# Performance work log

Hardware: AMD Instinct MI355X
Metric: run time of the kernel (lower is better)

The kernel has to match this reference:

```python
import jax, jax.numpy as jnp
import numpy as np

N = 5000
E = 160000
H = 6   # num_heads
D = 64  # out feats per head
IN = 131


def _gat_layer(h, W, al, ar, b, src, dst, activate):
    """DGL-style GATConv: fc -> edge attention -> edge softmax -> scatter sum."""
    n = h.shape[0]
    f = (h @ W).reshape(n, H, D)                      # [N,H,D]
    el = (f * al).sum(-1)                             # [N,H]
    er = (f * ar).sum(-1)                             # [N,H]
    e = jax.nn.leaky_relu(el[src] + er[dst], 0.2)     # [E,H]
    emax = jax.ops.segment_max(e, dst, num_segments=n)
    ex = jnp.exp(e - emax[dst])
    den = jax.ops.segment_sum(ex, dst, num_segments=n)
    alpha = ex / den[dst]                             # [E,H] edge softmax per dst
    out = jax.ops.segment_sum(f[src] * alpha[:, :, None], dst, num_segments=n)
    out = out + b.reshape(H, D)
    return jax.nn.elu(out) if activate else out


def setup_inputs() -> dict:
    ks = jax.random.split(jax.random.key(0), 24)
    s = 0.05
    inp = {
        "nfeats": jax.random.normal(ks[0], (N, IN), jnp.float32),
        "dis": jax.random.uniform(ks[1], (N, N), jnp.float32),
        "src": jax.random.randint(ks[2], (E,), 0, N),
        "dst": jax.random.randint(ks[3], (E,), 0, N),
    }
    dims_in = [IN, H * D, H * D, H * D]
    for l in range(4):
        inp[f"w{l}"] = jax.random.normal(ks[4 + 4 * l], (dims_in[l], H * D), jnp.float32) * s
        inp[f"al{l}"] = jax.random.normal(ks[5 + 4 * l], (H, D), jnp.float32) * s
        inp[f"ar{l}"] = jax.random.normal(ks[6 + 4 * l], (H, D), jnp.float32) * s
        inp[f"b{l}"] = jax.random.normal(ks[7 + 4 * l], (H * D,), jnp.float32) * s
    inp["pw"] = jax.random.normal(ks[20], (129,), jnp.float32) * s
    inp["pb"] = jax.random.normal(ks[21], (), jnp.float32) * s
    return inp


def reference(nfeats, dis, src, dst,
              w0, al0, ar0, b0, w1, al1, ar1, b1,
              w2, al2, ar2, b2, w3, al3, ar3, b3, pw, pb):
    n = nfeats.shape[0]
    h = nfeats
    h = _gat_layer(h, w0, al0, ar0, b0, src, dst, True).reshape(n, H * D)
    h = _gat_layer(h, w1, al1, ar1, b1, src, dst, True).reshape(n, H * D)
    h = _gat_layer(h, w2, al2, ar2, b2, src, dst, True).reshape(n, H * D)
    emb = _gat_layer(h, w3, al3, ar3, b3, src, dst, False).mean(axis=1)  # [N,64]
    # pair_emb[i,j] = [emb[j], emb[i], dis[i,j]] -> Linear(129,1) -> tanh
    s1 = emb @ pw[:D]        # coefficient on emb[j]
    s2 = emb @ pw[D:2 * D]   # coefficient on emb[i]
    OD = jnp.tanh(s2[:, None] + s1[None, :] + dis * pw[2 * D] + pb)
    return OD
```

## Files before the change

kernel.cpp:

```cpp
#include <hip/hip_runtime.h>
#include <math.h>

#define N_NODES 5000
#define E_EDGES 160000
#define H_HEADS 6
#define D_FEAT  64
#define IN_FEAT 131
#define HD      384
#define NC4     (N_NODES/4)
#define AGG_CAP 1024

typedef float vf4 __attribute__((ext_vector_type(4)));

__global__ void k_count(const int* __restrict__ dst, int* __restrict__ deg) {
    int e = blockIdx.x * blockDim.x + threadIdx.x;
    if (e < E_EDGES) atomicAdd(&deg[dst[e]], 1);
}

__global__ void k_scan(int* __restrict__ deg, int* __restrict__ row_ptr) {
    __shared__ int part[1024];
    const int T = 1024;
    int t = threadIdx.x;
    const int per = (N_NODES + T - 1) / T;
    int start = t * per;
    int s = 0;
    for (int i = 0; i < per; i++) {
        int idx = start + i;
        if (idx < N_NODES) s += deg[idx];
    }
    part[t] = s;
    __syncthreads();
    for (int off = 1; off < T; off <<= 1) {
        int v = (t >= off) ? part[t - off] : 0;
        __syncthreads();
        part[t] += v;
        __syncthreads();
    }
    int excl = (t == 0) ? 0 : part[t - 1];
    for (int i = 0; i < per; i++) {
        int idx = start + i;
        if (idx < N_NODES) {
            row_ptr[idx] = excl;
            excl += deg[idx];
            deg[idx] = 0;
        }
    }
    if (t == T - 1) row_ptr[N_NODES] = part[T - 1];
}

__global__ void k_fill(const int* __restrict__ src, const int* __restrict__ dst,
                       const int* __restrict__ row_ptr,
                       int* __restrict__ cursor, int* __restrict__ csrc) {
    int e = blockIdx.x * blockDim.x + threadIdx.x;
    if (e < E_EDGES) {
        int d = dst[e];
        int p = atomicAdd(&cursor[d], 1);
        csrc[row_ptr[d] + p] = src[e];
    }
}

__global__ __launch_bounds__(64, 8) void k_gemm(const float* __restrict__ A,
                                                const float* __restrict__ W,
                                                float* __restrict__ C, int M, int K) {
    const int BM = 32, BN = 32, BK = 32;
    __shared__ float As[BK][BM + 4];
    __shared__ float Bs[BK][BN + 4];
    int bx = blockIdx.x;
    int by = blockIdx.y;
    int tid = threadIdx.x;
    int tx = tid & 7, ty = tid >> 3;
    int rowBase = by * BM;
    int colBase = bx * BN;
    float acc[4][4] = {};
    const bool kvec = ((K & 3) == 0);
    for (int k0 = 0; k0 < K; k0 += BK) {
#pragma unroll
        for (int i = 0; i < 4; i++) {
            int m = (tid >> 3) + 8 * i;
            int gr = rowBase + m;
            int gk = k0 + (tid & 7) * 4;
            float4 v = {0.f, 0.f, 0.f, 0.f};
            if (gr < M) {
                if (kvec && gk + 3 < K) {
                    v = *(const float4*)(A + (size_t)gr * K + gk);
                } else {
                    float* vv = (float*)&v;
#pragma unroll
                    for (int q = 0; q < 4; q++)
                        if (gk + q < K) vv[q] = A[(size_t)gr * K + gk + q];
                }
            }
            int kk = (tid & 7) * 4;
            As[kk + 0][m] = v.x;
            As[kk + 1][m] = v.y;
            As[kk + 2][m] = v.z;
            As[kk + 3][m] = v.w;
        }
#pragma unroll
        for (int i = 0; i < 4; i++) {
            int kr = (tid >> 3) + 8 * i;
            int gk = k0 + kr;
            float4 v = {0.f, 0.f, 0.f, 0.f};
            if (gk < K) v = *(const float4*)(W + (size_t)gk * HD + colBase + (tid & 7) * 4);
            *(float4*)&Bs[kr][(tid & 7) * 4] = v;
        }
        __syncthreads();
#pragma unroll 8
        for (int k = 0; k < BK; k++) {
            float4 a = *(const float4*)&As[k][ty * 4];
            float4 b = *(const float4*)&Bs[k][tx * 4];
            const float* ap = (const float*)&a;
            const float* bp = (const float*)&b;
#pragma unroll
            for (int i = 0; i < 4; i++)
#pragma unroll
                for (int j = 0; j < 4; j++) acc[i][j] += ap[i] * bp[j];
        }
        __syncthreads();
    }
#pragma unroll
    for (int i = 0; i < 4; i++) {
        int gr = rowBase + ty * 4 + i;
        if (gr < M) {
            float4 v = {acc[i][0], acc[i][1], acc[i][2], acc[i][3]};
            *(float4*)(C + (size_t)gr * HD + colBase + tx * 4) = v;
        }
    }
}

__global__ void k_elr(const float* __restrict__ f, const float* __restrict__ al,
                      const float* __restrict__ ar, float* __restrict__ el,
                      float* __restrict__ er) {
    int wave = (blockIdx.x * blockDim.x + threadIdx.x) >> 6;
    int lane = threadIdx.x & 63;
    if (wave >= N_NODES * H_HEADS) return;
    int n = wave / H_HEADS, h = wave % H_HEADS;
    float v = f[n * HD + h * D_FEAT + lane];
    float pl = v * al[h * D_FEAT + lane];
    float pr = v * ar[h * D_FEAT + lane];
    for (int off = 32; off; off >>= 1) {
        pl += __shfl_down(pl, off);
        pr += __shfl_down(pr, off);
    }
    if (lane == 0) { el[wave] = pl; er[wave] = pr; }
}

__global__ __launch_bounds__(384) void k_agg(const float* __restrict__ f,
                                             const float* __restrict__ el,
                                             const float* __restrict__ er,
                                             const float* __restrict__ bias,
                                             const int* __restrict__ row_ptr,
                                             const int* __restrict__ csrc,
                                             float* __restrict__ out, int activate) {
    __shared__ int   s_src[AGG_CAP];
    __shared__ float s_x[H_HEADS][AGG_CAP];
    __shared__ float sh_inv[H_HEADS];
    int node = blockIdx.x;
    int t = threadIdx.x;
    int h = t >> 6, lane = t & 63;
    int r0 = row_ptr[node], r1 = row_ptr[node + 1];
    int deg = r1 - r0;
    int dcap = deg < AGG_CAP ? deg : AGG_CAP;
    float er_h = er[node * H_HEADS + h];

    for (int i = t; i < dcap; i += 384) s_src[i] = csrc[r0 + i];
    __syncthreads();

    float m = -1e30f;
    for (int i = lane; i < dcap; i += 64) {
        int s = s_src[i];
        float x = el[s * H_HEADS + h] + er_h;
        x = x >= 0.f ? x : 0.2f * x;
        s_x[h][i] = x;
        m = fmaxf(m, x);
    }
    for (int i = AGG_CAP + lane; i < deg; i += 64) {
        int s = csrc[r0 + i];
        float x = el[s * H_HEADS + h] + er_h;
        x = x >= 0.f ? x : 0.2f * x;
        m = fmaxf(m, x);
    }
    for (int off = 32; off; off >>= 1) m = fmaxf(m, __shfl_down(m, off));
    m = __shfl(m, 0);

    float ssum = 0.f;
    for (int i = lane; i < dcap; i += 64) {
        float w = __expf(s_x[h][i] - m);
        s_x[h][i] = w;
        ssum += w;
    }
    for (int i = AGG_CAP + lane; i < deg; i += 64) {
        int s = csrc[r0 + i];
        float x = el[s * H_HEADS + h] + er_h;
        x = x >= 0.f ? x : 0.2f * x;
        ssum += __expf(x - m);
    }
    for (int off = 32; off; off >>= 1) ssum += __shfl_down(ssum, off);
    if (lane == 0) sh_inv[h] = (ssum > 0.f) ? 1.f / ssum : 0.f;
    __syncthreads();
    float inv = sh_inv[h];

    const float* fh = f + h * D_FEAT + lane;
    float acc = 0.f;
    int i = 0;
    int lim = dcap & ~7;
    for (; i < lim; i += 8) {
        int s0 = s_src[i + 0], s1 = s_src[i + 1], s2 = s_src[i + 2], s3 = s_src[i + 3];
        int s4 = s_src[i + 4], s5 = s_src[i + 5], s6 = s_src[i + 6], s7 = s_src[i + 7];
        float f0 = fh[(size_t)s0 * HD], f1 = fh[(size_t)s1 * HD];
        float f2 = fh[(size_t)s2 * HD], f3 = fh[(size_t)s3 * HD];
        float f4 = fh[(size_t)s4 * HD], f5 = fh[(size_t)s5 * HD];
        float f6 = fh[(size_t)s6 * HD], f7 = fh[(size_t)s7 * HD];
        acc += s_x[h][i + 0] * f0;
        acc += s_x[h][i + 1] * f1;
        acc += s_x[h][i + 2] * f2;
        acc += s_x[h][i + 3] * f3;
        acc += s_x[h][i + 4] * f4;
        acc += s_x[h][i + 5] * f5;
        acc += s_x[h][i + 6] * f6;
        acc += s_x[h][i + 7] * f7;
    }
    for (; i < dcap; i++) {
        acc += s_x[h][i] * fh[(size_t)s_src[i] * HD];
    }
    for (i = AGG_CAP; i < deg; i++) {
        int s = csrc[r0 + i];
        float x = el[s * H_HEADS + h] + er_h;
        x = x >= 0.f ? x : 0.2f * x;
        acc += __expf(x - m) * fh[(size_t)s * HD];
    }
    float o = acc * inv + bias[h * D_FEAT + lane];
    if (activate) o = o > 0.f ? o : (__expf(o) - 1.f);
    out[node * HD + h * D_FEAT + lane] = o;
}

__global__ void k_embed(const float* __restrict__ h3, const float* __restrict__ pw,
                        float* __restrict__ s1, float* __restrict__ s2) {
    int wave = (blockIdx.x * blockDim.x + threadIdx.x) >> 6;
    int lane = threadIdx.x & 63;
    if (wave >= N_NODES) return;
    float s = 0.f;
#pragma unroll
    for (int hh = 0; hh < H_HEADS; hh++) s += h3[wave * HD + hh * D_FEAT + lane];
    s *= (1.f / 6.f);
    float p1 = s * pw[lane];
    float p2 = s * pw[D_FEAT + lane];
    for (int off = 32; off; off >>= 1) {
        p1 += __shfl_down(p1, off);
        p2 += __shfl_down(p2, off);
    }
    if (lane == 0) { s1[wave] = p1; s2[wave] = p2; }
}

__device__ __forceinline__ float fast_tanh(float z) {
    float t = __expf(-2.f * fabsf(z));
    float r = (1.f - t) / (1.f + t);
    return copysignf(r, z);
}

__global__ void k_pair(const vf4* __restrict__ dis, const float* __restrict__ s1,
                       const float* __restrict__ s2, const float* __restrict__ pw,
                       const float* __restrict__ pb, vf4* __restrict__ out) {
    const int total = N_NODES * NC4;
    float w = pw[2 * D_FEAT];
    float b = pb[0];
    for (int idx = blockIdx.x * blockDim.x + threadIdx.x; idx < total;
         idx += gridDim.x * blockDim.x) {
        int i = idx / NC4;
        int j4 = idx - i * NC4;
        vf4 dv = __builtin_nontemporal_load(&dis[idx]);
        float base = s2[i] + b;
        int j = j4 * 4;
        vf4 o;
        o.x = fast_tanh(base + s1[j + 0] + dv.x * w);
        o.y = fast_tanh(base + s1[j + 1] + dv.y * w);
        o.z = fast_tanh(base + s1[j + 2] + dv.z * w);
        o.w = fast_tanh(base + s1[j + 3] + dv.w * w);
        __builtin_nontemporal_store(o, &out[idx]);
    }
}

extern "C" void kernel_launch(void* const* d_in, const int* in_sizes, int n_in,
                              void* d_out, int out_size, void* d_ws, size_t ws_size,
                              hipStream_t stream) {
    const float* nfeats = (const float*)d_in[0];
    const float* dis    = (const float*)d_in[1];
    const int*   src    = (const int*)d_in[2];
    const int*   dst    = (const int*)d_in[3];
    const float* w[4]  = {(const float*)d_in[4],  (const float*)d_in[8],
                          (const float*)d_in[12], (const float*)d_in[16]};
    const float* al[4] = {(const float*)d_in[5],  (const float*)d_in[9],
                          (const float*)d_in[13], (const float*)d_in[17]};
    const float* ar[4] = {(const float*)d_in[6],  (const float*)d_in[10],
                          (const float*)d_in[14], (const float*)d_in[18]};
    const float* bs[4] = {(const float*)d_in[7],  (const float*)d_in[11],
                          (const float*)d_in[15], (const float*)d_in[19]};
    const float* pw = (const float*)d_in[20];
    const float* pb = (const float*)d_in[21];
    float* out = (float*)d_out;

    float* f    = (float*)d_ws;
    float* hbuf = f + N_NODES * HD;
    float* el   = hbuf + N_NODES * HD;
    float* er   = el + N_NODES * H_HEADS;
    float* s1   = er + N_NODES * H_HEADS;
    float* s2   = s1 + N_NODES;
    int* row_ptr = (int*)(s2 + N_NODES);
    int* cursor  = row_ptr + (N_NODES + 1);
    int* csrc    = cursor + N_NODES;

    (void)hipMemsetAsync(cursor, 0, N_NODES * sizeof(int), stream);
    k_count<<<(E_EDGES + 255) / 256, 256, 0, stream>>>(dst, cursor);
    k_scan<<<1, 1024, 0, stream>>>(cursor, row_ptr);
    k_fill<<<(E_EDGES + 255) / 256, 256, 0, stream>>>(src, dst, row_ptr, cursor, csrc);

    const float* hin = nfeats;
    for (int l = 0; l < 4; l++) {
        int K = (l == 0) ? IN_FEAT : HD;
        dim3 g(HD / 32, (N_NODES + 31) / 32);
        k_gemm<<<g, 64, 0, stream>>>(hin, w[l], f, N_NODES, K);
        k_elr<<<(N_NODES * H_HEADS + 3) / 4, 256, 0, stream>>>(f, al[l], ar[l], el, er);
        k_agg<<<N_NODES, 384, 0, stream>>>(f, el, er, bs[l], row_ptr, csrc, hbuf,
                                           (l < 3) ? 1 : 0);
        hin = hbuf;
    }
    k_embed<<<(N_NODES + 3) / 4, 256, 0, stream>>>(hbuf, pw, s1, s2);
    k_pair<<<4096, 256, 0, stream>>>((const vf4*)dis, s1, s2, pw, pb, (vf4*)out);
}
```

Before: 604.6 us.

## Use split-fp16 MFMA GEMM with fused attention-logit epilogue

Replaces the FP32 SIMT tiled GEMM with an MFMA 16x16x32 f16 kernel. Precision is recovered by splitting operands into hi/lo halves and doing three MFMAs per tile. The el/er attention dot products are folded into the GEMM epilogue, which removes the separate k_elr kernel. The aggregation kernel now also writes hi/lo f16 copies of the next layer's input, and weights are converted and transposed each call. The cost is extra conversion kernels, more workspace, and a small loss in accuracy from the split-f16 approximation.

```diff
diff --git a/kernel.cpp b/kernel.cpp
--- a/kernel.cpp
+++ b/kernel.cpp
@@ -9,8 +9,13 @@
 #define HD      384
 #define NC4     (N_NODES/4)
 #define AGG_CAP 1024
-
-typedef float vf4 __attribute__((ext_vector_type(4)));
+#define MPAD    5024
+#define KP0     160
+
+typedef float vf4   __attribute__((ext_vector_type(4)));
+typedef float f32x4 __attribute__((ext_vector_type(4)));
+typedef _Float16 h16;
+typedef _Float16 half8 __attribute__((ext_vector_type(8)));
 
 __global__ void k_count(const int* __restrict__ dst, int* __restrict__ deg) {
     int e = blockIdx.x * blockDim.x + threadIdx.x;
@@ -59,90 +64,97 @@
     }
 }
 
-__global__ __launch_bounds__(64, 8) void k_gemm(const float* __restrict__ A,
-                                                const float* __restrict__ W,
-                                                float* __restrict__ C, int M, int K) {
-    const int BM = 32, BN = 32, BK = 32;
-    __shared__ float As[BK][BM + 4];
-    __shared__ float Bs[BK][BN + 4];
-    int bx = blockIdx.x;
-    int by = blockIdx.y;
-    int tid = threadIdx.x;
-    int tx = tid & 7, ty = tid >> 3;
-    int rowBase = by * BM;
-    int colBase = bx * BN;
-    float acc[4][4] = {};
-    const bool kvec = ((K & 3) == 0);
-    for (int k0 = 0; k0 < K; k0 += BK) {
-#pragma unroll
-        for (int i = 0; i < 4; i++) {
-            int m = (tid >> 3) + 8 * i;
-            int gr = rowBase + m;
-            int gk = k0 + (tid & 7) * 4;
-            float4 v = {0.f, 0.f, 0.f, 0.f};
-            if (gr < M) {
-                if (kvec && gk + 3 < K) {
-                    v = *(const float4*)(A + (size_t)gr * K + gk);
-                } else {
-                    float* vv = (float*)&v;
-#pragma unroll
-                    for (int q = 0; q < 4; q++)
-                        if (gk + q < K) vv[q] = A[(size_t)gr * K + gk + q];
-                }
+__global__ void k_cvt_a0(const float* __restrict__ A, h16* __restrict__ hi,
+                         h16* __restrict__ lo) {
+    int idx = blockIdx.x * blockDim.x + threadIdx.x;
+    if (idx >= MPAD * KP0) return;
+    int r = idx / KP0, k = idx - r * KP0;
+    float v = (r < N_NODES && k < IN_FEAT) ? A[r * IN_FEAT + k] : 0.f;
+    h16 h = (h16)v;
+    hi[idx] = h;
+    lo[idx] = (h16)(v - (float)h);
+}
+
+__global__ void k_cvt_w(const float* __restrict__ W, h16* __restrict__ hi,
+                        h16* __restrict__ lo, int K, int KP) {
+    int idx = blockIdx.x * blockDim.x + threadIdx.x;
+    if (idx >= HD * KP) return;
+    int n = idx / KP, k = idx - n * KP;
+    float v = (k < K) ? W[(size_t)k * HD + n] : 0.f;
+    h16 h = (h16)v;
+    hi[idx] = h;
+    lo[idx] = (h16)(v - (float)h);
+}
+
+__global__ __launch_bounds__(64, 2) void k_gemm_mfma(
+        const h16* __restrict__ Ahi, const h16* __restrict__ Alo,
+        const h16* __restrict__ Wthi, const h16* __restrict__ Wtlo,
+        const float* __restrict__ al, const float* __restrict__ ar,
+        float* __restrict__ C, float* __restrict__ el, float* __restrict__ er,
+        int KP) {
+    int lane = threadIdx.x;
+    int h = blockIdx.x;
+    int rb = blockIdx.y * 32;
+    int cb = h * 64;
+    int l15 = lane & 15, lg = lane >> 4;
+    f32x4 acc[2][4] = {};
+
+    const h16* a0h = Ahi + (size_t)(rb + l15) * KP + (lg << 3);
+    const h16* a0l = Alo + (size_t)(rb + l15) * KP + (lg << 3);
+    const h16* a1h = a0h + (size_t)16 * KP;
+    const h16* a1l = a0l + (size_t)16 * KP;
+    const h16* bh = Wthi + (size_t)(cb + l15) * KP + (lg << 3);
+    const h16* bl = Wtlo + (size_t)(cb + l15) * KP + (lg << 3);
+
+#pragma unroll 2
+    for (int k0 = 0; k0 < KP; k0 += 32) {
+        half8 A0h = *(const half8*)(a0h + k0);
+        half8 A0l = *(const half8*)(a0l + k0);
+        half8 A1h = *(const half8*)(a1h + k0);
+        half8 A1l = *(const half8*)(a1l + k0);
+#pragma unroll
+        for (int t = 0; t < 4; t++) {
+            half8 Bh = *(const half8*)(bh + (size_t)t * 16 * KP + k0);
+            half8 Bl = *(const half8*)(bl + (size_t)t * 16 * KP + k0);
+            acc[0][t] = __builtin_amdgcn_mfma_f32_16x16x32_f16(A0h, Bh, acc[0][t], 0, 0, 0);
+            acc[0][t] = __builtin_amdgcn_mfma_f32_16x16x32_f16(A0l, Bh, acc[0][t], 0, 0, 0);
+            acc[0][t] = __builtin_amdgcn_mfma_f32_16x16x32_f16(A0h, Bl, acc[0][t], 0, 0, 0);
+            acc[1][t] = __builtin_amdgcn_mfma_f32_16x16x32_f16(A1h, Bh, acc[1][t], 0, 0, 0);
+            acc[1][t] = __builtin_amdgcn_mfma_f32_16x16x32_f16(A1l, Bh, acc[1][t], 0, 0, 0);
+            acc[1][t] = __builtin_amdgcn_mfma_f32_16x16x32_f16(A1h, Bl, acc[1][t], 0, 0, 0);
+        }
+    }
+
+    float alv[4], arv[4];
+#pragma unroll
+    for (int t = 0; t < 4; t++) {
+        alv[t] = al[h * D_FEAT + t * 16 + l15];
+        arv[t] = ar[h * D_FEAT + t * 16 + l15];
+    }
+#pragma unroll
+    for (int m = 0; m < 2; m++) {
+#pragma unroll
+        for (int r = 0; r < 4; r++) {
+            int grow = rb + m * 16 + lg * 4 + r;
+            float sl = 0.f, sr = 0.f;
+#pragma unroll
+            for (int t = 0; t < 4; t++) {
+                float v = acc[m][t][r];
+                if (grow < N_NODES) C[(size_t)grow * HD + cb + t * 16 + l15] = v;
+                sl += v * alv[t];
+                sr += v * arv[t];
             }
-            int kk = (tid & 7) * 4;
-            As[kk + 0][m] = v.x;
-            As[kk + 1][m] = v.y;
-            As[kk + 2][m] = v.z;
-            As[kk + 3][m] = v.w;
+#pragma unroll
+            for (int off = 1; off < 16; off <<= 1) {
+                sl += __shfl_xor(sl, off);
+                sr += __shfl_xor(sr, off);
+            }
+            if (l15 == 0 && grow < N_NODES) {
+                el[grow * H_HEADS + h] = sl;
+                er[grow * H_HEADS + h] = sr;
+            }
         }
-#pragma unroll
-        for (int i = 0; i < 4; i++) {
-            int kr = (tid >> 3) + 8 * i;
-            int gk = k0 + kr;
-            float4 v = {0.f, 0.f, 0.f, 0.f};
-            if (gk < K) v = *(const float4*)(W + (size_t)gk * HD + colBase + (tid & 7) * 4);
-            *(float4*)&Bs[kr][(tid & 7) * 4] = v;
-        }
-        __syncthreads();
-#pragma unroll 8
-        for (int k = 0; k < BK; k++) {
-            float4 a = *(const float4*)&As[k][ty * 4];
-            float4 b = *(const float4*)&Bs[k][tx * 4];
-            const float* ap = (const float*)&a;
-            const float* bp = (const float*)&b;
-#pragma unroll
-            for (int i = 0; i < 4; i++)
-#pragma unroll
-                for (int j = 0; j < 4; j++) acc[i][j] += ap[i] * bp[j];
-        }
-        __syncthreads();
-    }
-#pragma unroll
-    for (int i = 0; i < 4; i++) {
-        int gr = rowBase + ty * 4 + i;
-        if (gr < M) {
-            float4 v = {acc[i][0], acc[i][1], acc[i][2], acc[i][3]};
-            *(float4*)(C + (size_t)gr * HD + colBase + tx * 4) = v;
-        }
-    }
-}
-
-__global__ void k_elr(const float* __restrict__ f, const float* __restrict__ al,
-                      const float* __restrict__ ar, float* __restrict__ el,
-                      float* __restrict__ er) {
-    int wave = (blockIdx.x * blockDim.x + threadIdx.x) >> 6;
-    int lane = threadIdx.x & 63;
-    if (wave >= N_NODES * H_HEADS) return;
-    int n = wave / H_HEADS, h = wave % H_HEADS;
-    float v = f[n * HD + h * D_FEAT + lane];
-    float pl = v * al[h * D_FEAT + lane];
-    float pr = v * ar[h * D_FEAT + lane];
-    for (int off = 32; off; off >>= 1) {
-        pl += __shfl_down(pl, off);
-        pr += __shfl_down(pr, off);
-    }
-    if (lane == 0) { el[wave] = pl; er[wave] = pr; }
+    }
 }
 
 __global__ __launch_bounds__(384) void k_agg(const float* __restrict__ f,
@@ -151,7 +163,9 @@
                                              const float* __restrict__ bias,
                                              const int* __restrict__ row_ptr,
                                              const int* __restrict__ csrc,
-                                             float* __restrict__ out, int activate) {
+                                             float* __restrict__ out, int activate,
+                                             h16* __restrict__ nhi,
+                                             h16* __restrict__ nlo) {
     __shared__ int   s_src[AGG_CAP];
     __shared__ float s_x[H_HEADS][AGG_CAP];
     __shared__ float sh_inv[H_HEADS];
@@ -231,7 +245,13 @@
     }
     float o = acc * inv + bias[h * D_FEAT + lane];
     if (activate) o = o > 0.f ? o : (__expf(o) - 1.f);
-    out[node * HD + h * D_FEAT + lane] = o;
+    int oi = node * HD + h * D_FEAT + lane;
+    out[oi] = o;
+    if (nhi) {
+        h16 oh = (h16)o;
+        nhi[oi] = oh;
+        nlo[oi] = (h16)(o - (float)oh);
+    }
 }
 
 __global__ void k_embed(const float* __restrict__ h3, const float* __restrict__ pw,
@@ -308,21 +328,41 @@
     int* row_ptr = (int*)(s2 + N_NODES);
     int* cursor  = row_ptr + (N_NODES + 1);
     int* csrc    = cursor + N_NODES;
+    uintptr_t p = (uintptr_t)(csrc + E_EDGES);
+    p = (p + 15) & ~(uintptr_t)15;
+    h16* A0hi = (h16*)p;
+    h16* A0lo = A0hi + (size_t)MPAD * KP0;
+    h16* Athi = A0lo + (size_t)MPAD * KP0;
+    h16* Atlo = Athi + (size_t)MPAD * HD;
+    h16* Wthi = Atlo + (size_t)MPAD * HD;
+    h16* Wtlo = Wthi + (size_t)HD * HD;
 
     (void)hipMemsetAsync(cursor, 0, N_NODES * sizeof(int), stream);
     k_count<<<(E_EDGES + 255) / 256, 256, 0, stream>>>(dst, cursor);
     k_scan<<<1, 1024, 0, stream>>>(cursor, row_ptr);
     k_fill<<<(E_EDGES + 255) / 256, 256, 0, stream>>>(src, dst, row_ptr, cursor, csrc);
 
-    const float* hin = nfeats;
-    for (int l = 0; l < 4; l++) {
-        int K = (l == 0) ? IN_FEAT : HD;
-        dim3 g(HD / 32, (N_NODES + 31) / 32);
-        k_gemm<<<g, 64, 0, stream>>>(hin, w[l], f, N_NODES, K);
-        k_elr<<<(N_NODES * H_HEADS + 3) / 4, 256, 0, stream>>>(f, al[l], ar[l], el, er);
+    (void)hipMemsetAsync(Athi + (size_t)N_NODES * HD, 0,
+                         (size_t)(MPAD - N_NODES) * HD * sizeof(h16), stream);
+    (void)hipMemsetAsync(Atlo + (size_t)N_NODES * HD, 0,
+                         (size_t)(MPAD - N_NODES) * HD * sizeof(h16), stream);
+
+    dim3 gg(H_HEADS, (N_NODES + 31) / 32);
+
+    k_cvt_a0<<<(MPAD * KP0 + 255) / 256, 256, 0, stream>>>(nfeats, A0hi, A0lo);
+    k_cvt_w<<<(HD * KP0 + 255) / 256, 256, 0, stream>>>(w[0], Wthi, Wtlo, IN_FEAT, KP0);
+    k_gemm_mfma<<<gg, 64, 0, stream>>>(A0hi, A0lo, Wthi, Wtlo, al[0], ar[0],
+                                       f, el, er, KP0);
+    k_agg<<<N_NODES, 384, 0, stream>>>(f, el, er, bs[0], row_ptr, csrc, hbuf, 1,
+                                       Athi, Atlo);
+    for (int l = 1; l < 4; l++) {
+        k_cvt_w<<<(HD * HD + 255) / 256, 256, 0, stream>>>(w[l], Wthi, Wtlo, HD, HD);
+        k_gemm_mfma<<<gg, 64, 0, stream>>>(Athi, Atlo, Wthi, Wtlo, al[l], ar[l],
+                                           f, el, er, HD);
         k_agg<<<N_NODES, 384, 0, stream>>>(f, el, er, bs[l], row_ptr, csrc, hbuf,
-                                           (l < 3) ? 1 : 0);
-        hin = hbuf;
+                                           (l < 3) ? 1 : 0,
+                                           (l < 3) ? Athi : (h16*)nullptr,
+                                           (l < 3) ? Atlo : (h16*)nullptr);
     }
     k_embed<<<(N_NODES + 3) / 4, 256, 0, stream>>>(hbuf, pw, s1, s2);
     k_pair<<<4096, 256, 0, stream>>>((const vf4*)dis, s1, s2, pw, pb, (vf4*)out);
```

Measured after the change: 501.7 us. 17.0% less time.
